# Performance work log

Measured on AMD Instinct MI355X. Metric: run time of the kernel, lower is better.

The kernel has to match this reference:

```python
import jax, jax.numpy as jnp
import numpy as np

K = 4      # number of per-slot Linear layers (self.k)
H = 512    # hidden_dim
B = 4      # branching factor at every tree level (B >= K -> no padded slots)
T = 1024   # number of trees (roots)
D = 3      # pooled tree levels (= idx_matrix.shape[1] - 2)
N0 = T * B ** D  # 65536 leaves


def _make_level(n_in):
    """Replicates the torch order_matrix / pooling construction for groups of size B.
    order[m, i] = group_base + (pos_in_group + m) % B, then +1 for the zero pad row.
    seg[i] = group id (torch.repeat_interleave of counts)."""
    i = np.arange(n_in)
    base = (i // B) * B
    pos = i % B
    m = np.arange(K)[:, None]
    order = base[None, :] + (pos[None, :] + m) % B + 1  # [K, n_in], all valid since B >= K
    seg = i // B
    return order.astype(np.int32), seg.astype(np.int32)


def setup_inputs() -> dict:
    key = jax.random.key(0)
    ks = jax.random.split(key, 5)
    x = jax.random.normal(ks[0], (N0, H), jnp.float32)
    node_idx = jnp.arange(N0, dtype=jnp.int32)  # idx_matrix[:, -1]
    o1, s1 = _make_level(N0)
    o2, s2 = _make_level(N0 // B)
    o3, s3 = _make_level(N0 // B // B)
    Wz = jax.random.normal(ks[1], (K, H, H), jnp.float32) / np.sqrt(H)   # k slot Linears
    bz = jax.random.normal(ks[2], (K, H), jnp.float32) * 0.02
    Wzf = jax.random.normal(ks[3], (H, H), jnp.float32) / np.sqrt(H)     # z_final_layer
    bzf = jax.random.normal(ks[4], (H,), jnp.float32) * 0.02
    return dict(x=x, Wz=Wz, bz=bz, Wzf=Wzf, bzf=bzf, node_idx=node_idx,
                order1=jnp.asarray(o1), order2=jnp.asarray(o2), order3=jnp.asarray(o3),
                seg1=jnp.asarray(s1), seg2=jnp.asarray(s2), seg3=jnp.asarray(s3))


def _tree_layer(data, order, seg, num_seg, Wz, bz, Wzf, bzf):
    # prepend zero row so padded entries (order == 0) gather zeros
    padded = jnp.concatenate([jnp.zeros((1, data.shape[-1]), data.dtype), data], axis=0)
    emb = padded[order]                                    # [K, N, H] gather
    emb = jnp.einsum('knh,kjh->nkj', emb, Wz) + bz[None]   # per-slot Linear (x @ W.T + b)
    emb = jnp.where((order.T == 0)[..., None], jnp.zeros((), emb.dtype), emb)  # mask padded slots
    emb = emb.sum(axis=1)                                  # sum over K slots -> [N, H]
    emb = emb @ Wzf.T + bzf                                # z_final_layer
    return jax.ops.segment_sum(emb, seg, num_segments=num_seg)  # global_add_pool


def reference(x, Wz, bz, Wzf, bzf, node_idx, order1, order2, order3, seg1, seg2, seg3):
    data = x[node_idx]
    for order, seg in ((order1, seg1), (order2, seg2), (order3, seg3)):
        data = _tree_layer(data, order, seg, order.shape[1] // B, Wz, bz, Wzf, bzf)
    return data  # [T, H]
```

## Files before the change

### kernel.cpp

```cpp
#include <hip/hip_runtime.h>


#define HD 512

typedef __attribute__((ext_vector_type(8))) short bf16x8;
typedef __attribute__((ext_vector_type(4))) float f32x4;

struct __align__(16) MfmaSmem {
    unsigned short Ah[64][40];
    unsigned short Al[64][40];
    unsigned short Bh[64][40];
    unsigned short Bl[64][40];
};

template<bool BIAS>
__device__ __forceinline__
void mfma_gemm(const float* __restrict__ A, const float* __restrict__ Bt,
               float* __restrict__ C, const float* __restrict__ bias,
               float bscale, int i0, int j0, MfmaSmem& sm) {
    const int t = threadIdx.x;
    const int sr = t >> 2, sk = (t & 3) << 3;
    const int lane = t & 63, w = t >> 6;
    const int fm = lane & 15, fq = (lane >> 4) << 3;

    f32x4 acc[4] = {};

    for (int k0 = 0; k0 < HD; k0 += 32) {
        __syncthreads();
        {
            const float* ap = &A[(size_t)(i0 + sr) * HD + k0 + sk];
            float4 a0 = *(const float4*)ap, a1 = *(const float4*)(ap + 4);
            float f[8] = {a0.x, a0.y, a0.z, a0.w, a1.x, a1.y, a1.z, a1.w};
            bf16x8 hv, lv;
            #pragma unroll
            for (int i = 0; i < 8; ++i) {
                unsigned u = __float_as_uint(f[i]);
                hv[i] = (short)(u >> 16);
                float hi = __uint_as_float(u & 0xFFFF0000u);
                lv[i] = (short)(__float_as_uint(f[i] - hi) >> 16);
            }
            *(bf16x8*)&sm.Ah[sr][sk] = hv;
            *(bf16x8*)&sm.Al[sr][sk] = lv;
        }
        {
            const float* bp = &Bt[(size_t)(j0 + sr) * HD + k0 + sk];
            float4 b0 = *(const float4*)bp, b1 = *(const float4*)(bp + 4);
            float f[8] = {b0.x, b0.y, b0.z, b0.w, b1.x, b1.y, b1.z, b1.w};
            bf16x8 hv, lv;
            #pragma unroll
            for (int i = 0; i < 8; ++i) {
                unsigned u = __float_as_uint(f[i]);
                hv[i] = (short)(u >> 16);
                float hi = __uint_as_float(u & 0xFFFF0000u);
                lv[i] = (short)(__float_as_uint(f[i] - hi) >> 16);
            }
            *(bf16x8*)&sm.Bh[sr][sk] = hv;
            *(bf16x8*)&sm.Bl[sr][sk] = lv;
        }
        __syncthreads();

        bf16x8 ah = *(const bf16x8*)&sm.Ah[(w << 4) + fm][fq];
        bf16x8 al = *(const bf16x8*)&sm.Al[(w << 4) + fm][fq];
        #pragma unroll
        for (int ct = 0; ct < 4; ++ct) {
            bf16x8 bh = *(const bf16x8*)&sm.Bh[(ct << 4) + fm][fq];
            bf16x8 bl = *(const bf16x8*)&sm.Bl[(ct << 4) + fm][fq];
            acc[ct] = __builtin_amdgcn_mfma_f32_16x16x32_bf16(ah, bh, acc[ct], 0, 0, 0);
            acc[ct] = __builtin_amdgcn_mfma_f32_16x16x32_bf16(ah, bl, acc[ct], 0, 0, 0);
            acc[ct] = __builtin_amdgcn_mfma_f32_16x16x32_bf16(al, bh, acc[ct], 0, 0, 0);
        }
    }

    const int orow = i0 + (w << 4) + ((lane >> 4) << 2);
    #pragma unroll
    for (int ct = 0; ct < 4; ++ct) {
        const int col = j0 + (ct << 4) + fm;
        float bv = BIAS ? bscale * bias[col] : 0.f;
        #pragma unroll
        for (int r = 0; r < 4; ++r)
            C[(size_t)(orow + r) * HD + col] = acc[ct][r] + bv;
    }
}

union D1Smem {
    float  tp[64][68];
    float4 red[128];
};

__global__ __launch_bounds__(256) void kD1(
        const float* __restrict__ x, const float* __restrict__ Wz,
        const float* __restrict__ bz, const float* __restrict__ Wzf,
        const float* __restrict__ bzf,
        float* __restrict__ P3, float* __restrict__ WsumT, float* __restrict__ c0) {
    __shared__ D1Smem sm;
    const int b = blockIdx.x, t = threadIdx.x;
    if (b < 1024) {
        const int c = t & 127, h = t >> 7;
        const float4* xp = (const float4*)x + (size_t)b * 8192 + h * 4096 + c;
        float4 acc = make_float4(0.f, 0.f, 0.f, 0.f);
        for (int r = 0; r < 32; r += 4) {
            float4 v0 = xp[(r + 0) * 128], v1 = xp[(r + 1) * 128];
            float4 v2 = xp[(r + 2) * 128], v3 = xp[(r + 3) * 128];
            acc.x += (v0.x + v1.x) + (v2.x + v3.x);
            acc.y += (v0.y + v1.y) + (v2.y + v3.y);
            acc.z += (v0.z + v1.z) + (v2.z + v3.z);
            acc.w += (v0.w + v1.w) + (v2.w + v3.w);
        }
        if (h) sm.red[c] = acc;
        __syncthreads();
        if (!h) {
            float4 o = sm.red[c];
            acc.x += o.x; acc.y += o.y; acc.z += o.z; acc.w += o.w;
            ((float4*)P3)[b * 128 + c] = acc;
        }
    } else if (b < 1088) {
        const int bb = b - 1024;
        const int j0t = (bb >> 3) << 6, h0t = (bb & 7) << 6;
        const int rr = t >> 4, cc = (t & 15) << 2;
        #pragma unroll
        for (int p = 0; p < 4; ++p) {
            const float* wp = &Wz[(size_t)(j0t + rr + 16 * p) * HD + h0t + cc];
            float4 s = *(const float4*)wp;
            #pragma unroll
            for (int q = 1; q < 4; ++q) {
                float4 v = *(const float4*)(wp + q * 262144);
                s.x += v.x; s.y += v.y; s.z += v.z; s.w += v.w;
            }
            *(float4*)&sm.tp[rr + 16 * p][cc] = s;
        }
        __syncthreads();
        #pragma unroll
        for (int p = 0; p < 4; ++p) {
            const int hr = rr + 16 * p;
            float4 o = make_float4(sm.tp[cc + 0][hr], sm.tp[cc + 1][hr],
                                   sm.tp[cc + 2][hr], sm.tp[cc + 3][hr]);
            *(float4*)&WsumT[(size_t)(h0t + hr) * HD + j0t + cc] = o;
        }
    } else {
        const int lane = t & 63, w = t >> 6, hb = lane << 3;
        const int j = (b - 1088) * 4 + w;
        float4 s0 = *(const float4*)&bz[hb];
        float4 s1 = *(const float4*)&bz[hb + 4];
        #pragma unroll
        for (int q = 1; q < 4; ++q) {
            float4 t0 = *(const float4*)&bz[q * HD + hb];
            float4 t1 = *(const float4*)&bz[q * HD + hb + 4];
            s0.x += t0.x; s0.y += t0.y; s0.z += t0.z; s0.w += t0.w;
            s1.x += t1.x; s1.y += t1.y; s1.z += t1.z; s1.w += t1.w;
        }
        const float4* wr = (const float4*)&Wzf[(size_t)j * HD + hb];
        float4 w0 = wr[0], w1 = wr[1];
        float p = w0.x * s0.x + w0.y * s0.y + w0.z * s0.z + w0.w * s0.w
                + w1.x * s1.x + w1.y * s1.y + w1.z * s1.z + w1.w * s1.w;
        #pragma unroll
        for (int off = 32; off > 0; off >>= 1) p += __shfl_down(p, off);
        if (lane == 0) c0[j] = 4.f * (p + bzf[j]);
    }
}

__global__ __launch_bounds__(256) void kD2(
        const float* __restrict__ Wzf, const float* __restrict__ WsumT,
        float* __restrict__ M, float* __restrict__ MT) {
    __shared__ MfmaSmem sm;
    const int b = blockIdx.x;
    if (b < 64) {
        mfma_gemm<false>(Wzf, WsumT, M, nullptr, 0.f,
                         (b >> 3) << 6, (b & 7) << 6, sm);
    } else {
        const int bb = b - 64;
        mfma_gemm<false>(WsumT, Wzf, MT, nullptr, 0.f,
                         (bb >> 3) << 6, (bb & 7) << 6, sm);
    }
}

__global__ __launch_bounds__(256) void kD3(
        const float* __restrict__ P3, const float* __restrict__ M,
        const float* __restrict__ MT, const float* __restrict__ c0,
        float* __restrict__ Y1, float* __restrict__ M2, float* __restrict__ u) {
    __shared__ MfmaSmem sm;
    const int b = blockIdx.x, t = threadIdx.x;
    if (b < 128) {
        mfma_gemm<true>(P3, M, Y1, c0, 16.f, (b >> 3) << 6, (b & 7) << 6, sm);
    } else if (b < 192) {
        const int bb = b - 128;
        mfma_gemm<false>(M, MT, M2, nullptr, 0.f,
                         (bb >> 3) << 6, (bb & 7) << 6, sm);
    } else {
        const int lane = t & 63, w = t >> 6, hb = lane << 3;
        const int j = (b - 192) * 4 + w;
        const float4* mr = (const float4*)&M[(size_t)j * HD + hb];
        const float4* cr = (const float4*)&c0[hb];
        float4 m0 = mr[0], m1 = mr[1], q0 = cr[0], q1 = cr[1];
        float p = m0.x * q0.x + m0.y * q0.y + m0.z * q0.z + m0.w * q0.w
                + m1.x * q1.x + m1.y * q1.y + m1.z * q1.z + m1.w * q1.w;
        #pragma unroll
        for (int off = 32; off > 0; off >>= 1) p += __shfl_down(p, off);
        if (lane == 0) u[j] = 4.f * p + c0[j];
    }
}

__global__ __launch_bounds__(256) void kD4(
        const float* __restrict__ Y1, const float* __restrict__ M2,
        const float* __restrict__ u, float* __restrict__ out) {
    __shared__ MfmaSmem sm;
    const int b = blockIdx.x;
    mfma_gemm<true>(Y1, M2, out, u, 1.f, (b >> 3) << 6, (b & 7) << 6, sm);
}

extern "C" void kernel_launch(void* const* d_in, const int* in_sizes, int n_in,
                              void* d_out, int out_size, void* d_ws, size_t ws_size,
                              hipStream_t stream) {
    const float* x   = (const float*)d_in[0];
    const float* Wz  = (const float*)d_in[1];
    const float* bz  = (const float*)d_in[2];
    const float* Wzf = (const float*)d_in[3];
    const float* bzf = (const float*)d_in[4];
    float* out = (float*)d_out;

    float* ws    = (float*)d_ws;
    float* P3    = ws;
    float* Y1    = ws + 524288;
    float* WsumT = ws + 1048576;
    float* M     = ws + 1310720;
    float* MT    = ws + 1572864;
    float* M2    = ws + 1835008;
    float* c0    = ws + 2097152;
    float* u     = ws + 2097664;

    hipLaunchKernelGGL(kD1, dim3(1216), dim3(256), 0, stream,
                       x, Wz, bz, Wzf, bzf, P3, WsumT, c0);
    hipLaunchKernelGGL(kD2, dim3(128), dim3(256), 0, stream, Wzf, WsumT, M, MT);
    hipLaunchKernelGGL(kD3, dim3(320), dim3(256), 0, stream,
                       P3, M, MT, c0, Y1, M2, u);
    hipLaunchKernelGGL(kD4, dim3(128), dim3(256), 0, stream, Y1, M2, u, out);
}
```

Baseline: 263.9 us.

## Prefetch next K-tile in MFMA GEMM and split leaf reduction across two blocks

The split-bf16 MFMA GEMM now loads the next 32-wide K slice from global memory into registers while the current slice is being multiplied, so global latency overlaps with compute. The leaf-sum stage of kD1 is split into two blocks per tree with deeper unrolled loads, giving more parallelism and memory-level parallelism over the 128MB input. The two partial sums are combined by extra blocks added to kD2. This costs an extra workspace buffer and one more pass over the partials.

After: 254.1 us. 1.04x faster.

```diff
diff --git a/kernel.cpp b/kernel.cpp
--- a/kernel.cpp
+++ b/kernel.cpp
@@ -12,6 +12,18 @@
     unsigned short Bh[64][40];
     unsigned short Bl[64][40];
 };
+
+__device__ __forceinline__ void split8(const float4& v0, const float4& v1,
+                                       bf16x8& hv, bf16x8& lv) {
+    float f[8] = {v0.x, v0.y, v0.z, v0.w, v1.x, v1.y, v1.z, v1.w};
+    #pragma unroll
+    for (int i = 0; i < 8; ++i) {
+        unsigned u = __float_as_uint(f[i]);
+        hv[i] = (short)(u >> 16);
+        float hi = __uint_as_float(u & 0xFFFF0000u);
+        lv[i] = (short)(__float_as_uint(f[i] - hi) >> 16);
+    }
+}
 
 template<bool BIAS>
 __device__ __forceinline__
@@ -23,41 +35,31 @@
     const int lane = t & 63, w = t >> 6;
     const int fm = lane & 15, fq = (lane >> 4) << 3;
 
+    const float* ap = &A[(size_t)(i0 + sr) * HD + sk];
+    const float* bp = &Bt[(size_t)(j0 + sr) * HD + sk];
+    float4 a0 = *(const float4*)ap,      a1 = *(const float4*)(ap + 4);
+    float4 b0 = *(const float4*)bp,      b1 = *(const float4*)(bp + 4);
+
     f32x4 acc[4] = {};
 
-    for (int k0 = 0; k0 < HD; k0 += 32) {
-        __syncthreads();
-        {
-            const float* ap = &A[(size_t)(i0 + sr) * HD + k0 + sk];
-            float4 a0 = *(const float4*)ap, a1 = *(const float4*)(ap + 4);
-            float f[8] = {a0.x, a0.y, a0.z, a0.w, a1.x, a1.y, a1.z, a1.w};
-            bf16x8 hv, lv;
-            #pragma unroll
-            for (int i = 0; i < 8; ++i) {
-                unsigned u = __float_as_uint(f[i]);
-                hv[i] = (short)(u >> 16);
-                float hi = __uint_as_float(u & 0xFFFF0000u);
-                lv[i] = (short)(__float_as_uint(f[i] - hi) >> 16);
-            }
-            *(bf16x8*)&sm.Ah[sr][sk] = hv;
-            *(bf16x8*)&sm.Al[sr][sk] = lv;
-        }
-        {
-            const float* bp = &Bt[(size_t)(j0 + sr) * HD + k0 + sk];
-            float4 b0 = *(const float4*)bp, b1 = *(const float4*)(bp + 4);
-            float f[8] = {b0.x, b0.y, b0.z, b0.w, b1.x, b1.y, b1.z, b1.w};
-            bf16x8 hv, lv;
-            #pragma unroll
-            for (int i = 0; i < 8; ++i) {
-                unsigned u = __float_as_uint(f[i]);
-                hv[i] = (short)(u >> 16);
-                float hi = __uint_as_float(u & 0xFFFF0000u);
-                lv[i] = (short)(__float_as_uint(f[i] - hi) >> 16);
-            }
-            *(bf16x8*)&sm.Bh[sr][sk] = hv;
-            *(bf16x8*)&sm.Bl[sr][sk] = lv;
-        }
-        __syncthreads();
+    for (int it = 0; it < 16; ++it) {
+        __syncthreads();
+        bf16x8 hv, lv;
+        split8(a0, a1, hv, lv);
+        *(bf16x8*)&sm.Ah[sr][sk] = hv;
+        *(bf16x8*)&sm.Al[sr][sk] = lv;
+        split8(b0, b1, hv, lv);
+        *(bf16x8*)&sm.Bh[sr][sk] = hv;
+        *(bf16x8*)&sm.Bl[sr][sk] = lv;
+        __syncthreads();
+
+        if (it < 15) {
+            const int k0n = (it + 1) << 5;
+            a0 = *(const float4*)(ap + k0n);
+            a1 = *(const float4*)(ap + k0n + 4);
+            b0 = *(const float4*)(bp + k0n);
+            b1 = *(const float4*)(bp + k0n + 4);
+        }
 
         bf16x8 ah = *(const bf16x8*)&sm.Ah[(w << 4) + fm][fq];
         bf16x8 al = *(const bf16x8*)&sm.Al[(w << 4) + fm][fq];
@@ -91,30 +93,34 @@
         const float* __restrict__ x, const float* __restrict__ Wz,
         const float* __restrict__ bz, const float* __restrict__ Wzf,
         const float* __restrict__ bzf,
-        float* __restrict__ P3, float* __restrict__ WsumT, float* __restrict__ c0) {
+        float* __restrict__ part, float* __restrict__ WsumT, float* __restrict__ c0) {
     __shared__ D1Smem sm;
     const int b = blockIdx.x, t = threadIdx.x;
-    if (b < 1024) {
-        const int c = t & 127, h = t >> 7;
-        const float4* xp = (const float4*)x + (size_t)b * 8192 + h * 4096 + c;
+    if (b < 2048) {
+        const int tree = b >> 1, half = b & 1;
+        const int c = t & 127, sub = t >> 7;
+        const float4* xp = (const float4*)x + (size_t)tree * 8192
+                         + (half * 32 + sub * 16) * 128 + c;
         float4 acc = make_float4(0.f, 0.f, 0.f, 0.f);
-        for (int r = 0; r < 32; r += 4) {
-            float4 v0 = xp[(r + 0) * 128], v1 = xp[(r + 1) * 128];
-            float4 v2 = xp[(r + 2) * 128], v3 = xp[(r + 3) * 128];
-            acc.x += (v0.x + v1.x) + (v2.x + v3.x);
-            acc.y += (v0.y + v1.y) + (v2.y + v3.y);
-            acc.z += (v0.z + v1.z) + (v2.z + v3.z);
-            acc.w += (v0.w + v1.w) + (v2.w + v3.w);
-        }
-        if (h) sm.red[c] = acc;
-        __syncthreads();
-        if (!h) {
+        #pragma unroll
+        for (int g = 0; g < 2; ++g) {
+            float4 v[8];
+            #pragma unroll
+            for (int i = 0; i < 8; ++i) v[i] = xp[(size_t)(g * 8 + i) * 128];
+            #pragma unroll
+            for (int i = 0; i < 8; ++i) {
+                acc.x += v[i].x; acc.y += v[i].y; acc.z += v[i].z; acc.w += v[i].w;
+            }
+        }
+        if (sub) sm.red[c] = acc;
+        __syncthreads();
+        if (!sub) {
             float4 o = sm.red[c];
             acc.x += o.x; acc.y += o.y; acc.z += o.z; acc.w += o.w;
-            ((float4*)P3)[b * 128 + c] = acc;
-        }
-    } else if (b < 1088) {
-        const int bb = b - 1024;
+            ((float4*)part)[b * 128 + c] = acc;
+        }
+    } else if (b < 2112) {
+        const int bb = b - 2048;
         const int j0t = (bb >> 3) << 6, h0t = (bb & 7) << 6;
         const int rr = t >> 4, cc = (t & 15) << 2;
         #pragma unroll
@@ -138,7 +144,7 @@
         }
     } else {
         const int lane = t & 63, w = t >> 6, hb = lane << 3;
-        const int j = (b - 1088) * 4 + w;
+        const int j = (b - 2112) * 4 + w;
         float4 s0 = *(const float4*)&bz[hb];
         float4 s1 = *(const float4*)&bz[hb + 4];
         #pragma unroll
@@ -160,16 +166,30 @@
 
 __global__ __launch_bounds__(256) void kD2(
         const float* __restrict__ Wzf, const float* __restrict__ WsumT,
-        float* __restrict__ M, float* __restrict__ MT) {
+        const float* __restrict__ part,
+        float* __restrict__ M, float* __restrict__ MT, float* __restrict__ P3) {
     __shared__ MfmaSmem sm;
-    const int b = blockIdx.x;
+    const int b = blockIdx.x, t = threadIdx.x;
     if (b < 64) {
         mfma_gemm<false>(Wzf, WsumT, M, nullptr, 0.f,
                          (b >> 3) << 6, (b & 7) << 6, sm);
-    } else {
+    } else if (b < 128) {
         const int bb = b - 64;
         mfma_gemm<false>(WsumT, Wzf, MT, nullptr, 0.f,
                          (bb >> 3) << 6, (bb & 7) << 6, sm);
+    } else {
+        const int gid = (b - 128) * 256 + t;
+        const float4* p4 = (const float4*)part;
+        float4* o4 = (float4*)P3;
+        #pragma unroll
+        for (int h = 0; h < 2; ++h) {
+            const int i = gid + h * 65536;
+            const int tree = i >> 7, c = i & 127;
+            float4 pa = p4[(size_t)(2 * tree) * 128 + c];
+            float4 pb = p4[(size_t)(2 * tree + 1) * 128 + c];
+            pa.x += pb.x; pa.y += pb.y; pa.z += pb.z; pa.w += pb.w;
+            o4[i] = pa;
+        }
     }
 }
 
@@ -224,12 +244,14 @@
     float* M     = ws + 1310720;
     float* MT    = ws + 1572864;
     float* M2    = ws + 1835008;
-    float* c0    = ws + 2097152;
-    float* u     = ws + 2097664;
-
-    hipLaunchKernelGGL(kD1, dim3(1216), dim3(256), 0, stream,
-                       x, Wz, bz, Wzf, bzf, P3, WsumT, c0);
-    hipLaunchKernelGGL(kD2, dim3(128), dim3(256), 0, stream, Wzf, WsumT, M, MT);
+    float* part  = ws + 2097152;
+    float* c0    = ws + 3145728;
+    float* u     = ws + 3146240;
+
+    hipLaunchKernelGGL(kD1, dim3(2240), dim3(256), 0, stream,
+                       x, Wz, bz, Wzf, bzf, part, WsumT, c0);
+    hipLaunchKernelGGL(kD2, dim3(384), dim3(256), 0, stream,
+                       Wzf, WsumT, part, M, MT, P3);
     hipLaunchKernelGGL(kD3, dim3(320), dim3(256), 0, stream,
                        P3, M, MT, c0, Y1, M2, u);
     hipLaunchKernelGGL(kD4, dim3(128), dim3(256), 0, stream, Y1, M2, u, out);
```
